# Optimization experiments

Hardware: AMD Instinct MI355X
Metric: run time of the kernel (lower is better)

Reference implementation:

```python
import jax, jax.numpy as jnp
import numpy as np

ALPHA = 0.2  # LeakyReLU negative slope


def setup_inputs() -> dict:
    key = jax.random.key(0)
    k1, k2, k3, k4 = jax.random.split(key, 4)
    B, T, D_in, H, S = 32, 1024, 64, 64, 2
    embedding = jax.random.normal(k1, (B, T, D_in), dtype=jnp.float32)
    x = jax.random.normal(k2, (S * B, T, D_in), dtype=jnp.float32)
    # xavier_uniform-ish scale for params
    W = jax.random.normal(k3, (D_in, H), dtype=jnp.float32) * (1.414 * np.sqrt(2.0 / (D_in + H)))
    a = jax.random.normal(k4, (2 * H, 1), dtype=jnp.float32) * (1.414 * np.sqrt(2.0 / (2 * H + 1)))
    return {"embedding": embedding, "x": x, "W": W, "a": a, "input_size": S}


def reference(embedding, x, W, a, input_size):
    # embedding: [B, T, D_in], W: [D_in, H], a: [2H, 1], x: [S*B, T, D_in]
    H = W.shape[1]
    h = jnp.einsum("btd,dh->bth", embedding, W)          # [B, T, H]
    a1 = a[:H, 0]                                        # attends to h_i (query side)
    a2 = a[H:, 0]                                        # attends to h_j (key side)
    f1 = h @ a1                                          # [B, T]
    f2 = h @ a2                                          # [B, T]
    # e_ij = leakyrelu(a1.h_i + a2.h_j) -- avoids materializing [B,T,T,2H]
    e = jax.nn.leaky_relu(f1[:, :, None] + f2[:, None, :], negative_slope=ALPHA)  # [B, T, T]
    attn = jax.nn.softmax(e, axis=2)                     # [B, T, T]
    attn_tiled = jnp.tile(attn, (input_size, 1, 1))      # [S*B, T, T] (dropout: eval mode, identity)
    out = jnp.einsum("bij,bjd->bid", attn_tiled, x)      # [S*B, T, D_in]
    return out
```

## Files before the change

kernel.cpp:

```cpp
#include <hip/hip_runtime.h>

typedef float  f32x4 __attribute__((ext_vector_type(4)));
typedef _Float16 h16x8 __attribute__((ext_vector_type(8)));
typedef _Float16 h16x2 __attribute__((ext_vector_type(2)));
typedef unsigned uintx2 __attribute__((ext_vector_type(2)));

#define LOG2E 1.4426950408889634f
#define ALPHA 0.2f

__device__ __forceinline__ float fexp2(float v) {
#if __has_builtin(__builtin_amdgcn_exp2f)
  return __builtin_amdgcn_exp2f(v);
#else
  return exp2f(v);
#endif
}

__global__ __launch_bounds__(256) void fkern(
    const float* __restrict__ emb, const float* __restrict__ W,
    const float* __restrict__ a, float* __restrict__ f1, float* __restrict__ f2)
{
  __shared__ float Ws[64 * 65];
  __shared__ float w1s[64], w2s[64];
  const int t = threadIdx.x;
#pragma unroll
  for (int i = 0; i < 16; ++i) {
    const int idx = i * 256 + t;
    Ws[(idx >> 6) * 65 + (idx & 63)] = W[idx];
  }
  __syncthreads();
  if (t < 128) {
    const int d = t & 63;
    const float* av = a + (t >> 6) * 64;
    float s = 0.f;
#pragma unroll
    for (int h = 0; h < 64; ++h) s = fmaf(Ws[d * 65 + h], av[h], s);
    if (t < 64) w1s[d] = s; else w2s[d] = s;
  }
  __syncthreads();
  const int R = blockIdx.x * 64 + (t >> 2);
  const int q = t & 3;
  const f32x4* er = (const f32x4*)(emb + (size_t)R * 64 + q * 16);
  float s1 = 0.f, s2 = 0.f;
#pragma unroll
  for (int r = 0; r < 4; ++r) {
    f32x4 v = er[r];
#pragma unroll
    for (int c = 0; c < 4; ++c) {
      s1 = fmaf(v[c], w1s[q * 16 + r * 4 + c], s1);
      s2 = fmaf(v[c], w2s[q * 16 + r * 4 + c], s2);
    }
  }
  s1 += __shfl_xor(s1, 1); s1 += __shfl_xor(s1, 2);
  s2 += __shfl_xor(s2, 1); s2 += __shfl_xor(s2, 2);
  if (q == 0) { f1[R] = s1 * LOG2E; f2[R] = s2 * LOG2E; }
}

__global__ __launch_bounds__(1024, 1) void attn_main(
    const float* __restrict__ x, const float* __restrict__ f1g,
    const float* __restrict__ f2g, float* __restrict__ out)
{
  __shared__ __attribute__((aligned(16))) _Float16 Xt[2][128 * 128];
  __shared__ float e1s[1024], e2s[1024];
  __shared__ float red[16];

  const int t    = threadIdx.x;
  const int wid  = t >> 6;
  const int lane = t & 63;
  const int l15  = lane & 15;
  const int g    = lane >> 4;
  const int wc   = wid & 1;
  const int wr   = wid >> 1;
  const int b    = blockIdx.x & 31;
  const int brow = (blockIdx.x >> 5) * 128;

  const int R2 = g >> 1, u2 = g & 1;

  f32x4 rv[4];

  auto stage_loads = [&](int kc) {
#pragma unroll
    for (int c = 0; c < 4; ++c) {
      const int h = c >> 1;
      const int j = (c & 1) * 64 + wid * 4 + g;
      const float* p = x + (size_t)(b + 32 * h) * 65536
                         + (size_t)(kc * 128 + j) * 64 + l15 * 4;
      rv[c] = *(const f32x4*)p;
    }
  };
  auto stage_writes = [&](int buf) {
#pragma unroll
    for (int c = 0; c < 4; ++c) {
      f32x4 v = rv[c];
      float e0 = __shfl_xor(R2 ? v[0] : v[2], 32);
      float e1 = __shfl_xor(R2 ? v[1] : v[3], 32);
      if (R2) { v[0] = e0; v[1] = e1; } else { v[2] = e0; v[3] = e1; }
      float q0 = __shfl_xor(u2 ? v[0] : v[1], 16);
      float q1 = __shfl_xor(u2 ? v[2] : v[3], 16);
      if (u2) { v[0] = q0; v[2] = q1; } else { v[1] = q0; v[3] = q1; }
      uintx2 w;
      w[0] = __builtin_bit_cast(unsigned, __builtin_amdgcn_cvt_pkrtz(v[0], v[1]));
      w[1] = __builtin_bit_cast(unsigned, __builtin_amdgcn_cvt_pkrtz(v[2], v[3]));
      const int row = (c >> 1) * 64 + l15 * 4 + g;
      const int k8  = (c & 1) * 8 + (wr >> 0 ? 0 : 0) + (wid >> 1);
      const int kb  = k8 ^ (row & 7);
      *(uintx2*)&Xt[buf][row * 128 + kb * 8 + (wid & 1) * 4] = w;
    }
  };

  stage_loads(0);

  {
    const float v = f2g[b * 1024 + t];
    e1s[t] = fexp2(v);
    e2s[t] = fexp2(ALPHA * v);
    float m = v;
#pragma unroll
    for (int off = 1; off < 64; off <<= 1) m = fmaxf(m, __shfl_xor(m, off));
    if (lane == 0) red[wid] = m;
  }
  const float f1v = f1g[b * 1024 + brow + wr * 16 + l15];
  __syncthreads();
  float mf2 = red[0];
#pragma unroll
  for (int i = 1; i < 16; ++i) mf2 = fmaxf(mf2, red[i]);
  const float u  = f1v + mf2;
  const float mL = fmaxf(u, ALPHA * u);
  const float CA = fexp2(f1v - mL);
  const float CB = fexp2(fmaf(ALPHA, f1v, -mL));
  stage_writes(0);
  __syncthreads();

  f32x4 acc[4] = {};
  f32x4 accz = {};
  h16x8 ones;
#pragma unroll
  for (int i = 0; i < 8; ++i) ones[i] = (_Float16)1.0f;

  const int l7 = l15 & 7;

  for (int kc = 0; kc < 8; ++kc) {
    const int buf = kc & 1;
    if (kc < 7) stage_loads(kc + 1);
#pragma unroll
    for (int ks = 0; ks < 4; ++ks) {
      const int jb = kc * 128 + ks * 32 + g * 8;
      f32x4 e1a = *(const f32x4*)(e1s + jb);
      f32x4 e1b = *(const f32x4*)(e1s + jb + 4);
      f32x4 e2a = *(const f32x4*)(e2s + jb);
      f32x4 e2b = *(const f32x4*)(e2s + jb + 4);
      float ev1[8], ev2[8];
#pragma unroll
      for (int i = 0; i < 4; ++i) {
        ev1[i] = e1a[i]; ev1[4 + i] = e1b[i];
        ev2[i] = e2a[i]; ev2[4 + i] = e2b[i];
      }
      h16x8 a0;
#pragma unroll
      for (int jj = 0; jj < 4; ++jj) {
        float p0 = fmaxf(CA * ev1[2 * jj],     CB * ev2[2 * jj]);
        float p1 = fmaxf(CA * ev1[2 * jj + 1], CB * ev2[2 * jj + 1]);
        h16x2 pk = __builtin_bit_cast(h16x2, __builtin_amdgcn_cvt_pkrtz(p0, p1));
        a0[2 * jj] = pk[0]; a0[2 * jj + 1] = pk[1];
      }
#pragma unroll
      for (int nf = 0; nf < 4; ++nf) {
        const int row = wc * 64 + nf * 16 + l15;
        const int kb  = (ks * 4 + g) ^ l7;
        h16x8 bf = *(const h16x8*)&Xt[buf][row * 128 + kb * 8];
        acc[nf] = __builtin_amdgcn_mfma_f32_16x16x32_f16(a0, bf, acc[nf], 0, 0, 0);
      }
      accz = __builtin_amdgcn_mfma_f32_16x16x32_f16(a0, ones, accz, 0, 0, 0);
    }
    if (kc < 7) stage_writes(buf ^ 1);
    __syncthreads();
  }

  float rz[4];
#pragma unroll
  for (int r = 0; r < 4; ++r) rz[r] = 1.0f / accz[r];
  const int i0 = brow + wr * 16;
  const int bo = b + 32 * wc;
  float* op = out + (size_t)bo * 65536;
#pragma unroll
  for (int nf = 0; nf < 4; ++nf) {
    const int n = nf * 16 + l15;
#pragma unroll
    for (int r = 0; r < 4; ++r) {
      op[(size_t)(i0 + g * 4 + r) * 64 + n] = acc[nf][r] * rz[r];
    }
  }
}

extern "C" void kernel_launch(void* const* d_in, const int* in_sizes, int n_in,
                              void* d_out, int out_size, void* d_ws, size_t ws_size,
                              hipStream_t stream) {
  const float* emb = (const float*)d_in[0];
  const float* x   = (const float*)d_in[1];
  const float* W   = (const float*)d_in[2];
  const float* a   = (const float*)d_in[3];
  float* f1 = (float*)d_ws;
  float* f2 = f1 + 32 * 1024;
  fkern<<<512, 256, 0, stream>>>(emb, W, a, f1, f2);
  attn_main<<<256, 1024, 0, stream>>>(x, f1, f2, (float*)d_out);
}
```

Before: 40.82 us.

## Retile attention waves to 32x32 and compute exp2 per element from f2

Each wave now covers a 32-row by 32-column output tile (two A fragments times two B fragments) instead of 16x64. Every B fragment loaded from LDS therefore feeds two MFMAs, which cuts LDS reads per MFMA. The precomputed exp2(f2) tables are replaced by storing raw f2 and evaluating exp2(max(A+f, alpha*f+B)) per element. This trades the table reads and multiplies for more transcendental instructions, and the A-side work per wave doubles. A second row-sum MFMA per k-step is added as well.

```diff
diff --git a/kernel.cpp b/kernel.cpp
--- a/kernel.cpp
+++ b/kernel.cpp
@@ -61,7 +61,7 @@
     const float* __restrict__ f2g, float* __restrict__ out)
 {
   __shared__ __attribute__((aligned(16))) _Float16 Xt[2][128 * 128];
-  __shared__ float e1s[1024], e2s[1024];
+  __shared__ float f2s[1024];
   __shared__ float red[16];
 
   const int t    = threadIdx.x;
@@ -69,12 +69,13 @@
   const int lane = t & 63;
   const int l15  = lane & 15;
   const int g    = lane >> 4;
-  const int wc   = wid & 1;
-  const int wr   = wid >> 1;
+  const int l7   = lane & 7;
+  const int wc2  = wid & 3;
+  const int wr2  = wid >> 2;
   const int b    = blockIdx.x & 31;
   const int brow = (blockIdx.x >> 5) * 128;
 
-  const int R2 = g >> 1, u2 = g & 1;
+  const int R2 = g >> 1, u2g = g & 1;
 
   f32x4 rv[4];
 
@@ -95,14 +96,14 @@
       float e0 = __shfl_xor(R2 ? v[0] : v[2], 32);
       float e1 = __shfl_xor(R2 ? v[1] : v[3], 32);
       if (R2) { v[0] = e0; v[1] = e1; } else { v[2] = e0; v[3] = e1; }
-      float q0 = __shfl_xor(u2 ? v[0] : v[1], 16);
-      float q1 = __shfl_xor(u2 ? v[2] : v[3], 16);
-      if (u2) { v[0] = q0; v[2] = q1; } else { v[1] = q0; v[3] = q1; }
+      float q0 = __shfl_xor(u2g ? v[0] : v[1], 16);
+      float q1 = __shfl_xor(u2g ? v[2] : v[3], 16);
+      if (u2g) { v[0] = q0; v[2] = q1; } else { v[1] = q0; v[3] = q1; }
       uintx2 w;
       w[0] = __builtin_bit_cast(unsigned, __builtin_amdgcn_cvt_pkrtz(v[0], v[1]));
       w[1] = __builtin_bit_cast(unsigned, __builtin_amdgcn_cvt_pkrtz(v[2], v[3]));
       const int row = (c >> 1) * 64 + l15 * 4 + g;
-      const int k8  = (c & 1) * 8 + (wr >> 0 ? 0 : 0) + (wid >> 1);
+      const int k8  = (c & 1) * 8 + (wid >> 1);
       const int kb  = k8 ^ (row & 7);
       *(uintx2*)&Xt[buf][row * 128 + kb * 8 + (wid & 1) * 4] = w;
     }
@@ -112,32 +113,31 @@
 
   {
     const float v = f2g[b * 1024 + t];
-    e1s[t] = fexp2(v);
-    e2s[t] = fexp2(ALPHA * v);
+    f2s[t] = v;
     float m = v;
 #pragma unroll
     for (int off = 1; off < 64; off <<= 1) m = fmaxf(m, __shfl_xor(m, off));
     if (lane == 0) red[wid] = m;
   }
-  const float f1v = f1g[b * 1024 + brow + wr * 16 + l15];
+  const float f1a = f1g[b * 1024 + brow + wr2 * 32 + l15];
+  const float f1b = f1g[b * 1024 + brow + wr2 * 32 + 16 + l15];
   __syncthreads();
   float mf2 = red[0];
 #pragma unroll
   for (int i = 1; i < 16; ++i) mf2 = fmaxf(mf2, red[i]);
-  const float u  = f1v + mf2;
-  const float mL = fmaxf(u, ALPHA * u);
-  const float CA = fexp2(f1v - mL);
-  const float CB = fexp2(fmaf(ALPHA, f1v, -mL));
+  float A0, B0, A1, B1;
+  { const float u = f1a + mf2; const float mL = fmaxf(u, ALPHA * u);
+    A0 = f1a - mL; B0 = fmaf(ALPHA, f1a, -mL); }
+  { const float u = f1b + mf2; const float mL = fmaxf(u, ALPHA * u);
+    A1 = f1b - mL; B1 = fmaf(ALPHA, f1b, -mL); }
   stage_writes(0);
   __syncthreads();
 
-  f32x4 acc[4] = {};
-  f32x4 accz = {};
+  f32x4 acc[2][2] = {};
+  f32x4 accz[2] = {};
   h16x8 ones;
 #pragma unroll
   for (int i = 0; i < 8; ++i) ones[i] = (_Float16)1.0f;
-
-  const int l7 = l15 & 7;
 
   for (int kc = 0; kc < 8; ++kc) {
     const int buf = kc & 1;
@@ -145,49 +145,53 @@
 #pragma unroll
     for (int ks = 0; ks < 4; ++ks) {
       const int jb = kc * 128 + ks * 32 + g * 8;
-      f32x4 e1a = *(const f32x4*)(e1s + jb);
-      f32x4 e1b = *(const f32x4*)(e1s + jb + 4);
-      f32x4 e2a = *(const f32x4*)(e2s + jb);
-      f32x4 e2b = *(const f32x4*)(e2s + jb + 4);
-      float ev1[8], ev2[8];
-#pragma unroll
-      for (int i = 0; i < 4; ++i) {
-        ev1[i] = e1a[i]; ev1[4 + i] = e1b[i];
-        ev2[i] = e2a[i]; ev2[4 + i] = e2b[i];
+      f32x4 f2a = *(const f32x4*)(f2s + jb);
+      f32x4 f2b = *(const f32x4*)(f2s + jb + 4);
+      float fv[8];
+#pragma unroll
+      for (int i = 0; i < 4; ++i) { fv[i] = f2a[i]; fv[4 + i] = f2b[i]; }
+      h16x8 a0, a1;
+#pragma unroll
+      for (int jj = 0; jj < 4; ++jj) {
+        const float fA = fv[2 * jj], fB = fv[2 * jj + 1];
+        float p00 = fexp2(fmaxf(A0 + fA, fmaf(ALPHA, fA, B0)));
+        float p01 = fexp2(fmaxf(A0 + fB, fmaf(ALPHA, fB, B0)));
+        h16x2 pk0 = __builtin_bit_cast(h16x2, __builtin_amdgcn_cvt_pkrtz(p00, p01));
+        a0[2 * jj] = pk0[0]; a0[2 * jj + 1] = pk0[1];
+        float p10 = fexp2(fmaxf(A1 + fA, fmaf(ALPHA, fA, B1)));
+        float p11 = fexp2(fmaxf(A1 + fB, fmaf(ALPHA, fB, B1)));
+        h16x2 pk1 = __builtin_bit_cast(h16x2, __builtin_amdgcn_cvt_pkrtz(p10, p11));
+        a1[2 * jj] = pk1[0]; a1[2 * jj + 1] = pk1[1];
       }
-      h16x8 a0;
-#pragma unroll
-      for (int jj = 0; jj < 4; ++jj) {
-        float p0 = fmaxf(CA * ev1[2 * jj],     CB * ev2[2 * jj]);
-        float p1 = fmaxf(CA * ev1[2 * jj + 1], CB * ev2[2 * jj + 1]);
-        h16x2 pk = __builtin_bit_cast(h16x2, __builtin_amdgcn_cvt_pkrtz(p0, p1));
-        a0[2 * jj] = pk[0]; a0[2 * jj + 1] = pk[1];
+      const int kb = ((ks * 4 + g) ^ l7) * 8;
+#pragma unroll
+      for (int n2 = 0; n2 < 2; ++n2) {
+        const int row = wc2 * 32 + n2 * 16 + l15;
+        h16x8 bf = *(const h16x8*)&Xt[buf][row * 128 + kb];
+        acc[0][n2] = __builtin_amdgcn_mfma_f32_16x16x32_f16(a0, bf, acc[0][n2], 0, 0, 0);
+        acc[1][n2] = __builtin_amdgcn_mfma_f32_16x16x32_f16(a1, bf, acc[1][n2], 0, 0, 0);
       }
-#pragma unroll
-      for (int nf = 0; nf < 4; ++nf) {
-        const int row = wc * 64 + nf * 16 + l15;
-        const int kb  = (ks * 4 + g) ^ l7;
-        h16x8 bf = *(const h16x8*)&Xt[buf][row * 128 + kb * 8];
-        acc[nf] = __builtin_amdgcn_mfma_f32_16x16x32_f16(a0, bf, acc[nf], 0, 0, 0);
-      }
-      accz = __builtin_amdgcn_mfma_f32_16x16x32_f16(a0, ones, accz, 0, 0, 0);
+      accz[0] = __builtin_amdgcn_mfma_f32_16x16x32_f16(a0, ones, accz[0], 0, 0, 0);
+      accz[1] = __builtin_amdgcn_mfma_f32_16x16x32_f16(a1, ones, accz[1], 0, 0, 0);
     }
     if (kc < 7) stage_writes(buf ^ 1);
     __syncthreads();
   }
 
-  float rz[4];
-#pragma unroll
-  for (int r = 0; r < 4; ++r) rz[r] = 1.0f / accz[r];
-  const int i0 = brow + wr * 16;
-  const int bo = b + 32 * wc;
-  float* op = out + (size_t)bo * 65536;
-#pragma unroll
-  for (int nf = 0; nf < 4; ++nf) {
-    const int n = nf * 16 + l15;
-#pragma unroll
-    for (int r = 0; r < 4; ++r) {
-      op[(size_t)(i0 + g * 4 + r) * 64 + n] = acc[nf][r] * rz[r];
+  const int i0 = brow + wr2 * 32;
+#pragma unroll
+  for (int rr = 0; rr < 2; ++rr) {
+    f32x4 rzv;
+#pragma unroll
+    for (int r = 0; r < 4; ++r) rzv[r] = 1.0f / accz[rr][r];
+#pragma unroll
+    for (int n2 = 0; n2 < 2; ++n2) {
+      const int n  = wc2 * 32 + n2 * 16 + l15;
+      const int bo = b + ((n >= 64) ? 32 : 0);
+      float* op = out + (size_t)bo * 65536 + (n & 63);
+#pragma unroll
+      for (int r = 0; r < 4; ++r)
+        op[(size_t)(i0 + rr * 16 + g * 4 + r) * 64] = acc[rr][n2][r] * rzv[r];
     }
   }
 }
```

Result: slower. 49.13 us (+20.3%).
